# Kernel optimization log

Measured on AMD Instinct MI355X. Metric: run time of the kernel, lower is better.

## Reference

```python
import jax, jax.numpy as jnp
import numpy as np

N_NODES = 100000
N_EDGES = 600000
D = 128
BN_EPS = 1e-5


def setup_inputs() -> dict:
    key = jax.random.key(0)
    k = jax.random.split(key, 4)
    x = jax.random.normal(k[0], (N_NODES, D), dtype=jnp.float32)
    edge_index = jax.random.randint(k[1], (2, N_EDGES), 0, N_NODES, dtype=jnp.int32)
    W = jax.random.normal(k[2], (D, D), dtype=jnp.float32) * 0.05  # GCNConv weight
    b = jnp.zeros((D,), dtype=jnp.float32)                          # GCNConv bias
    gamma = jnp.ones((D,), dtype=jnp.float32)                       # BatchNorm weight
    beta = jnp.zeros((D,), dtype=jnp.float32)                       # BatchNorm bias
    return {"x": x, "edge_index": edge_index, "W": W, "b": b, "gamma": gamma, "beta": beta}


def reference(x, edge_index, W, b, gamma, beta):
    N = x.shape[0]
    # GCNConv: h = D^{-1/2} (A + I) D^{-1/2} (x W) + b
    h = x @ W  # [N, D]
    self_loops = jnp.arange(N, dtype=edge_index.dtype)
    src = jnp.concatenate([edge_index[0], self_loops])  # message source j
    dst = jnp.concatenate([edge_index[1], self_loops])  # aggregation target i
    deg = jax.ops.segment_sum(jnp.ones_like(dst, dtype=h.dtype), dst, num_segments=N)
    dinv = jax.lax.rsqrt(deg)  # deg >= 1 thanks to self-loops
    norm = dinv[src] * dinv[dst]  # [E+N]
    out = jax.ops.segment_sum(h[src] * norm[:, None], dst, num_segments=N) + b
    # BatchNorm (training-mode batch stats over nodes) + ReLU
    mean = jnp.mean(out, axis=0)
    var = jnp.mean((out - mean) ** 2, axis=0)
    out = (out - mean) * jax.lax.rsqrt(var + BN_EPS) * gamma + beta
    out = jax.nn.relu(out)
    # residual (in_ch == out_ch -> identity)
    return out + x
```

## Files before the change

kernel.cpp:

```cpp
#include <hip/hip_runtime.h>

#define NN 100000
#define NE 600000
#define DD 128
#define BN_EPS 1e-5f
#define NB1 391
#define NCV 12500
#define NFB 2344
#define NBLK 1563

typedef __attribute__((ext_vector_type(8))) short bf16x8;
typedef __attribute__((ext_vector_type(4))) float f32x4;

static __device__ __forceinline__ unsigned short f2bf(float f) {
    unsigned u = __float_as_uint(f);
    unsigned r = (u + 0x7FFFu + ((u >> 16) & 1u)) >> 16;
    return (unsigned short)r;
}
static __device__ __forceinline__ float bflo(unsigned v) { return __uint_as_float(v << 16); }
static __device__ __forceinline__ float bfhi(unsigned v) { return __uint_as_float(v & 0xFFFF0000u); }

__global__ __launch_bounds__(256) void k_init(int* __restrict__ cnt,
                                              float* __restrict__ stats,
                                              const float* __restrict__ W,
                                              unsigned short* __restrict__ Wt) {
    int i = blockIdx.x * 256 + threadIdx.x;
    if (i < NN) cnt[i] = 0;
    if (i < 256) stats[i] = 0.0f;
    if (i < DD * DD) {
        int k = i >> 7, c = i & 127;
        Wt[c * DD + k] = f2bf(W[i]);
    }
}

__global__ __launch_bounds__(256) void k_count(const int* __restrict__ dst,
                                               int* __restrict__ cnt) {
    int e = blockIdx.x * 256 + threadIdx.x;
    if (e < NE) atomicAdd(&cnt[dst[e]], 1);
}

__global__ __launch_bounds__(256) void k_scan1(const int* __restrict__ cnt,
                                               int* __restrict__ offs,
                                               int* __restrict__ bsum) {
    __shared__ int tmp[256];
    int tid = threadIdx.x;
    int i = blockIdx.x * 256 + tid;
    int v = (i < NN) ? (cnt[i] + 1) : 0;
    tmp[tid] = v;
    __syncthreads();
    #pragma unroll
    for (int d = 1; d < 256; d <<= 1) {
        int t = (tid >= d) ? tmp[tid - d] : 0;
        __syncthreads();
        tmp[tid] += t;
        __syncthreads();
    }
    if (i < NN) offs[i] = tmp[tid] - v;
    if (tid == 255) bsum[blockIdx.x] = tmp[255];
}

__global__ __launch_bounds__(512) void k_scan2(int* __restrict__ bsum) {
    __shared__ int tmp[512];
    int tid = threadIdx.x;
    int v = (tid < NB1) ? bsum[tid] : 0;
    tmp[tid] = v;
    __syncthreads();
    #pragma unroll
    for (int d = 1; d < 512; d <<= 1) {
        int t = (tid >= d) ? tmp[tid - d] : 0;
        __syncthreads();
        tmp[tid] += t;
        __syncthreads();
    }
    if (tid < NB1) bsum[tid] = tmp[tid] - v;
}

__global__ __launch_bounds__(256) void k_scan3(int* __restrict__ offs,
                                               const int* __restrict__ bsum,
                                               const int* __restrict__ cnt,
                                               int* __restrict__ cur,
                                               float* __restrict__ dinv,
                                               int* __restrict__ srcs) {
    int i = blockIdx.x * 256 + threadIdx.x;
    if (i < NN) {
        int o = offs[i] + bsum[blockIdx.x];
        offs[i] = o;
        dinv[i] = rsqrtf((float)(cnt[i] + 1));
        srcs[o] = i;
        cur[i]  = o + 1;
        if (i == 0) offs[NN] = NE + NN;
    }
}

__global__ __launch_bounds__(256) void k_cvfill(const float* __restrict__ x,
                                                const float* __restrict__ dinv,
                                                unsigned short* __restrict__ xn,
                                                const int* __restrict__ src,
                                                const int* __restrict__ dst,
                                                int* __restrict__ cur,
                                                int* __restrict__ srcs) {
    int bid = blockIdx.x;
    if (bid < NFB) {
        int e = bid * 256 + threadIdx.x;
        if (e < NE) {
            int s = src[e], t = dst[e];
            int slot = atomicAdd(&cur[t], 1);
            srcs[slot] = s;
        }
    } else {
        int r  = (bid - NFB) * 8 + (threadIdx.x >> 5);
        int c4 = threadIdx.x & 31;
        float di = dinv[r];
        float4 v = ((const float4*)x)[(size_t)r * 32 + c4];
        unsigned p0 = ((unsigned)f2bf(v.y * di) << 16) | f2bf(v.x * di);
        unsigned p1 = ((unsigned)f2bf(v.w * di) << 16) | f2bf(v.z * di);
        ((uint2*)xn)[(size_t)r * 32 + c4] = make_uint2(p0, p1);
    }
}

__global__ __launch_bounds__(256) void k_gather(const int* __restrict__ offs,
                                                const int* __restrict__ srcs,
                                                const unsigned short* __restrict__ xn,
                                                const float* __restrict__ dinv,
                                                const float* __restrict__ b,
                                                const unsigned short* __restrict__ Wt,
                                                float* __restrict__ out,
                                                float* __restrict__ partial) {
    __shared__ uint4 Wl4[2048];
    __shared__ float lsum[4][128], lss[4][128];
    const int tid  = threadIdx.x;
    const int wid  = tid >> 6;
    const int lane = tid & 63;
    const int lm   = lane & 15;
    const int lk   = lane >> 4;
    char* Wl = (char*)Wl4;

    #pragma unroll
    for (int it = 0; it < 8; ++it) {
        int chunk = it * 256 + tid;
        int row = chunk >> 4, c16 = chunk & 15;
        uint4 v = *(const uint4*)(Wt + row * DD + c16 * 8);
        *(uint4*)(Wl + row * 256 + ((c16 ^ (row & 7)) << 4)) = v;
    }
    float bb[8];
    #pragma unroll
    for (int nt = 0; nt < 8; ++nt) bb[nt] = b[nt * 16 + lm];
    __syncthreads();

    const int nbase = (blockIdx.x * 4 + wid) * 16;
    float s8[8], ss8[8];
    #pragma unroll
    for (int j = 0; j < 8; ++j) { s8[j] = 0.0f; ss8[j] = 0.0f; }

    if (nbase < NN) {
        int   ol = offs[nbase + (lane <= 16 ? lane : 16)];
        float dv = (lane < 16) ? dinv[nbase + lane] : 0.0f;
        int   beg = __shfl(ol, lm);
        int   n   = __shfl(ol, lm + 1) - beg;
        float di  = __shfl(dv, lm);
        const uint4* xn4 = (const uint4*)xn;

        float acc[4][8];
        #pragma unroll
        for (int ks = 0; ks < 4; ++ks)
            #pragma unroll
            for (int j = 0; j < 8; ++j) acc[ks][j] = 0.0f;

        int k = 0;
        for (; k + 2 <= n; k += 2) {
            int s0 = srcs[beg + k];
            int s1 = srcs[beg + k + 1];
            uint4 v0[4], v1[4];
            #pragma unroll
            for (int ks = 0; ks < 4; ++ks) v0[ks] = xn4[(size_t)s0 * 16 + ks * 4 + lk];
            #pragma unroll
            for (int ks = 0; ks < 4; ++ks) v1[ks] = xn4[(size_t)s1 * 16 + ks * 4 + lk];
            #pragma unroll
            for (int ks = 0; ks < 4; ++ks) {
                acc[ks][0] += bflo(v0[ks].x) + bflo(v1[ks].x);
                acc[ks][1] += bfhi(v0[ks].x) + bfhi(v1[ks].x);
                acc[ks][2] += bflo(v0[ks].y) + bflo(v1[ks].y);
                acc[ks][3] += bfhi(v0[ks].y) + bfhi(v1[ks].y);
                acc[ks][4] += bflo(v0[ks].z) + bflo(v1[ks].z);
                acc[ks][5] += bfhi(v0[ks].z) + bfhi(v1[ks].z);
                acc[ks][6] += bflo(v0[ks].w) + bflo(v1[ks].w);
                acc[ks][7] += bfhi(v0[ks].w) + bfhi(v1[ks].w);
            }
        }
        if (k < n) {
            int s0 = srcs[beg + k];
            #pragma unroll
            for (int ks = 0; ks < 4; ++ks) {
                uint4 v = xn4[(size_t)s0 * 16 + ks * 4 + lk];
                acc[ks][0] += bflo(v.x); acc[ks][1] += bfhi(v.x);
                acc[ks][2] += bflo(v.y); acc[ks][3] += bfhi(v.y);
                acc[ks][4] += bflo(v.z); acc[ks][5] += bfhi(v.z);
                acc[ks][6] += bflo(v.w); acc[ks][7] += bfhi(v.w);
            }
        }

        bf16x8 a[4];
        #pragma unroll
        for (int ks = 0; ks < 4; ++ks)
            #pragma unroll
            for (int j = 0; j < 8; ++j) a[ks][j] = (short)f2bf(acc[ks][j] * di);

        f32x4 dacc[8];
        #pragma unroll
        for (int nt = 0; nt < 8; ++nt) dacc[nt] = (f32x4){0.f, 0.f, 0.f, 0.f};
        #pragma unroll
        for (int ks = 0; ks < 4; ++ks)
            #pragma unroll
            for (int nt = 0; nt < 8; ++nt) {
                int brow = nt * 16 + lm;
                bf16x8 bfr = *(const bf16x8*)(Wl + brow * 256 + ((ks * 64 + lk * 16) ^ ((brow & 7) << 4)));
                dacc[nt] = __builtin_amdgcn_mfma_f32_16x16x32_bf16(a[ks], bfr, dacc[nt], 0, 0, 0);
            }

        #pragma unroll
        for (int nt = 0; nt < 8; ++nt)
            #pragma unroll
            for (int r = 0; r < 4; ++r) {
                float val = dacc[nt][r] + bb[nt];
                out[(size_t)(nbase + lk * 4 + r) * DD + nt * 16 + lm] = val;
                s8[nt] += val; ss8[nt] += val * val;
            }
    }

    #pragma unroll
    for (int nt = 0; nt < 8; ++nt) {
        s8[nt]  += __shfl_xor(s8[nt], 16);  s8[nt]  += __shfl_xor(s8[nt], 32);
        ss8[nt] += __shfl_xor(ss8[nt], 16); ss8[nt] += __shfl_xor(ss8[nt], 32);
    }
    if (lk == 0) {
        #pragma unroll
        for (int nt = 0; nt < 8; ++nt) {
            lsum[wid][nt * 16 + lm] = s8[nt];
            lss[wid][nt * 16 + lm]  = ss8[nt];
        }
    }
    __syncthreads();
    if (tid < 128) {
        float a = lsum[0][tid] + lsum[1][tid] + lsum[2][tid] + lsum[3][tid];
        float c = lss[0][tid]  + lss[1][tid]  + lss[2][tid]  + lss[3][tid];
        partial[(size_t)blockIdx.x * 256 + tid]       = a;
        partial[(size_t)blockIdx.x * 256 + 128 + tid] = c;
    }
}

__global__ __launch_bounds__(256) void k_red(const float* __restrict__ partial,
                                             float* __restrict__ stats) {
    int tid = threadIdx.x;
    float a = 0.0f;
    for (int r = blockIdx.x; r < NBLK; r += 64)
        a += partial[(size_t)r * 256 + tid];
    unsafeAtomicAdd(&stats[tid], a);
}

__global__ __launch_bounds__(256) void k_final(float* __restrict__ out,
                                               const float* __restrict__ x,
                                               const float* __restrict__ gamma,
                                               const float* __restrict__ beta,
                                               const float* __restrict__ stats) {
    int idx = blockIdx.x * 256 + threadIdx.x;
    if (idx >= NN * DD / 4) return;
    int c4 = idx & 31;

    const float invN = 1.0f / (float)NN;
    float4 sm  = ((const float4*)stats)[c4];
    float4 sq  = ((const float4*)stats)[32 + c4];
    float4 g   = ((const float4*)gamma)[c4];
    float4 be  = ((const float4*)beta)[c4];
    float4 v   = ((float4*)out)[idx];
    float4 xr  = ((const float4*)x)[idx];

    float m0 = sm.x * invN, m1 = sm.y * invN, m2 = sm.z * invN, m3 = sm.w * invN;
    float r0 = rsqrtf(sq.x * invN - m0 * m0 + BN_EPS);
    float r1 = rsqrtf(sq.y * invN - m1 * m1 + BN_EPS);
    float r2 = rsqrtf(sq.z * invN - m2 * m2 + BN_EPS);
    float r3 = rsqrtf(sq.w * invN - m3 * m3 + BN_EPS);

    float4 o;
    o.x = fmaxf((v.x - m0) * r0 * g.x + be.x, 0.0f) + xr.x;
    o.y = fmaxf((v.y - m1) * r1 * g.y + be.y, 0.0f) + xr.y;
    o.z = fmaxf((v.z - m2) * r2 * g.z + be.z, 0.0f) + xr.z;
    o.w = fmaxf((v.w - m3) * r3 * g.w + be.w, 0.0f) + xr.w;
    ((float4*)out)[idx] = o;
}

extern "C" void kernel_launch(void* const* d_in, const int* in_sizes, int n_in,
                              void* d_out, int out_size, void* d_ws, size_t ws_size,
                              hipStream_t stream) {
    const float* x     = (const float*)d_in[0];
    const int*   ei    = (const int*)d_in[1];
    const float* W     = (const float*)d_in[2];
    const float* b     = (const float*)d_in[3];
    const float* gamma = (const float*)d_in[4];
    const float* beta  = (const float*)d_in[5];
    float*       out   = (float*)d_out;

    char*  base = (char*)d_ws;
    size_t off  = 0;
    auto carve = [&](size_t bytes) -> void* {
        void* p = base + off;
        off = (off + bytes + 255) & ~(size_t)255;
        return p;
    };
    unsigned short* xn    = (unsigned short*)carve((size_t)NN * DD * 2);
    float*          dinv  = (float*)carve((size_t)NN * 4);
    float*          stats = (float*)carve(256 * 4);
    int*            cnt   = (int*)carve((size_t)NN * 4);
    int*            offs  = (int*)carve((size_t)(NN + 1) * 4);
    int*            cur   = (int*)carve((size_t)NN * 4);
    int*            bsum  = (int*)carve(2048);
    int*            srcs  = (int*)carve((size_t)(NE + NN) * 4);
    unsigned short* Wt    = (unsigned short*)carve(DD * DD * 2);
    float*          partial = (float*)carve((size_t)NBLK * 256 * 4);

    const int* src = ei;
    const int* dst = ei + NE;

    k_init   <<<NB1, 256, 0, stream>>>(cnt, stats, W, Wt);
    k_count  <<<(NE + 255) / 256, 256, 0, stream>>>(dst, cnt);
    k_scan1  <<<NB1, 256, 0, stream>>>(cnt, offs, bsum);
    k_scan2  <<<1, 512, 0, stream>>>(bsum);
    k_scan3  <<<NB1, 256, 0, stream>>>(offs, bsum, cnt, cur, dinv, srcs);
    k_cvfill <<<NFB + NCV, 256, 0, stream>>>(x, dinv, xn, src, dst, cur, srcs);
    k_gather <<<NBLK, 256, 0, stream>>>(offs, srcs, xn, dinv, b, Wt, out, partial);
    k_red    <<<64, 256, 0, stream>>>(partial, stats);
    k_final  <<<(NN * DD / 4 + 255) / 256, 256, 0, stream>>>(out, x, gamma, beta, stats);
}
```

Measured before the change: 159.3 us.

## Use persistent dynamic tile scheduling in gather and precompute edge ranks for CSR fill

The gather kernel becomes persistent: 1280 blocks whose waves pull 16-node tiles from a global atomic counter until all tiles are done. This is meant to balance uneven degree distributions and cut the number of per-block W-tile loads into LDS. The count kernel now records each edge's rank from its degree atomic, so the CSR fill writes slots directly without a second atomic pass. That removes the cur array but adds a rank array write and read. The stats scratch reuses the W LDS buffer behind an extra barrier.

```diff
diff --git a/kernel.cpp b/kernel.cpp
--- a/kernel.cpp
+++ b/kernel.cpp
@@ -7,7 +7,8 @@
 #define NB1 391
 #define NCV 12500
 #define NFB 2344
-#define NBLK 1563
+#define NBLK 1280
+#define NTILES 6250
 
 typedef __attribute__((ext_vector_type(8))) short bf16x8;
 typedef __attribute__((ext_vector_type(4))) float f32x4;
@@ -22,11 +23,13 @@
 
 __global__ __launch_bounds__(256) void k_init(int* __restrict__ cnt,
                                               float* __restrict__ stats,
+                                              int* __restrict__ ctr,
                                               const float* __restrict__ W,
                                               unsigned short* __restrict__ Wt) {
     int i = blockIdx.x * 256 + threadIdx.x;
     if (i < NN) cnt[i] = 0;
     if (i < 256) stats[i] = 0.0f;
+    if (i == 0) *ctr = 0;
     if (i < DD * DD) {
         int k = i >> 7, c = i & 127;
         Wt[c * DD + k] = f2bf(W[i]);
@@ -34,9 +37,10 @@
 }
 
 __global__ __launch_bounds__(256) void k_count(const int* __restrict__ dst,
-                                               int* __restrict__ cnt) {
+                                               int* __restrict__ cnt,
+                                               int* __restrict__ rank) {
     int e = blockIdx.x * 256 + threadIdx.x;
-    if (e < NE) atomicAdd(&cnt[dst[e]], 1);
+    if (e < NE) rank[e] = atomicAdd(&cnt[dst[e]], 1);
 }
 
 __global__ __launch_bounds__(256) void k_scan1(const int* __restrict__ cnt,
@@ -78,7 +82,6 @@
 __global__ __launch_bounds__(256) void k_scan3(int* __restrict__ offs,
                                                const int* __restrict__ bsum,
                                                const int* __restrict__ cnt,
-                                               int* __restrict__ cur,
                                                float* __restrict__ dinv,
                                                int* __restrict__ srcs) {
     int i = blockIdx.x * 256 + threadIdx.x;
@@ -87,7 +90,6 @@
         offs[i] = o;
         dinv[i] = rsqrtf((float)(cnt[i] + 1));
         srcs[o] = i;
-        cur[i]  = o + 1;
         if (i == 0) offs[NN] = NE + NN;
     }
 }
@@ -97,15 +99,15 @@
                                                 unsigned short* __restrict__ xn,
                                                 const int* __restrict__ src,
                                                 const int* __restrict__ dst,
-                                                int* __restrict__ cur,
+                                                const int* __restrict__ rank,
+                                                const int* __restrict__ offs,
                                                 int* __restrict__ srcs) {
     int bid = blockIdx.x;
     if (bid < NFB) {
         int e = bid * 256 + threadIdx.x;
         if (e < NE) {
-            int s = src[e], t = dst[e];
-            int slot = atomicAdd(&cur[t], 1);
-            srcs[slot] = s;
+            int t = dst[e];
+            srcs[offs[t] + 1 + rank[e]] = src[e];
         }
     } else {
         int r  = (bid - NFB) * 8 + (threadIdx.x >> 5);
@@ -124,10 +126,10 @@
                                                 const float* __restrict__ dinv,
                                                 const float* __restrict__ b,
                                                 const unsigned short* __restrict__ Wt,
+                                                int* __restrict__ ctr,
                                                 float* __restrict__ out,
                                                 float* __restrict__ partial) {
     __shared__ uint4 Wl4[2048];
-    __shared__ float lsum[4][128], lss[4][128];
     const int tid  = threadIdx.x;
     const int wid  = tid >> 6;
     const int lane = tid & 63;
@@ -147,18 +149,23 @@
     for (int nt = 0; nt < 8; ++nt) bb[nt] = b[nt * 16 + lm];
     __syncthreads();
 
-    const int nbase = (blockIdx.x * 4 + wid) * 16;
     float s8[8], ss8[8];
     #pragma unroll
     for (int j = 0; j < 8; ++j) { s8[j] = 0.0f; ss8[j] = 0.0f; }
-
-    if (nbase < NN) {
+    const uint4* xn4 = (const uint4*)xn;
+
+    for (;;) {
+        int tile = 0;
+        if (lane == 0) tile = atomicAdd(ctr, 1);
+        tile = __shfl(tile, 0);
+        if (tile >= NTILES) break;
+        const int nbase = tile * 16;
+
         int   ol = offs[nbase + (lane <= 16 ? lane : 16)];
         float dv = (lane < 16) ? dinv[nbase + lane] : 0.0f;
         int   beg = __shfl(ol, lm);
         int   n   = __shfl(ol, lm + 1) - beg;
         float di  = __shfl(dv, lm);
-        const uint4* xn4 = (const uint4*)xn;
 
         float acc[4][8];
         #pragma unroll
@@ -232,17 +239,19 @@
         s8[nt]  += __shfl_xor(s8[nt], 16);  s8[nt]  += __shfl_xor(s8[nt], 32);
         ss8[nt] += __shfl_xor(ss8[nt], 16); ss8[nt] += __shfl_xor(ss8[nt], 32);
     }
+    __syncthreads();
+    float* sp = (float*)Wl4;
     if (lk == 0) {
         #pragma unroll
         for (int nt = 0; nt < 8; ++nt) {
-            lsum[wid][nt * 16 + lm] = s8[nt];
-            lss[wid][nt * 16 + lm]  = ss8[nt];
+            sp[wid * 128 + nt * 16 + lm]       = s8[nt];
+            sp[512 + wid * 128 + nt * 16 + lm] = ss8[nt];
         }
     }
     __syncthreads();
     if (tid < 128) {
-        float a = lsum[0][tid] + lsum[1][tid] + lsum[2][tid] + lsum[3][tid];
-        float c = lss[0][tid]  + lss[1][tid]  + lss[2][tid]  + lss[3][tid];
+        float a = sp[tid] + sp[128 + tid] + sp[256 + tid] + sp[384 + tid];
+        float c = sp[512 + tid] + sp[640 + tid] + sp[768 + tid] + sp[896 + tid];
         partial[(size_t)blockIdx.x * 256 + tid]       = a;
         partial[(size_t)blockIdx.x * 256 + 128 + tid] = c;
     }
@@ -311,22 +320,23 @@
     float*          stats = (float*)carve(256 * 4);
     int*            cnt   = (int*)carve((size_t)NN * 4);
     int*            offs  = (int*)carve((size_t)(NN + 1) * 4);
-    int*            cur   = (int*)carve((size_t)NN * 4);
+    int*            rank  = (int*)carve((size_t)NE * 4);
     int*            bsum  = (int*)carve(2048);
     int*            srcs  = (int*)carve((size_t)(NE + NN) * 4);
     unsigned short* Wt    = (unsigned short*)carve(DD * DD * 2);
+    int*            ctr   = (int*)carve(256);
     float*          partial = (float*)carve((size_t)NBLK * 256 * 4);
 
     const int* src = ei;
     const int* dst = ei + NE;
 
-    k_init   <<<NB1, 256, 0, stream>>>(cnt, stats, W, Wt);
-    k_count  <<<(NE + 255) / 256, 256, 0, stream>>>(dst, cnt);
+    k_init   <<<NB1, 256, 0, stream>>>(cnt, stats, ctr, W, Wt);
+    k_count  <<<(NE + 255) / 256, 256, 0, stream>>>(dst, cnt, rank);
     k_scan1  <<<NB1, 256, 0, stream>>>(cnt, offs, bsum);
     k_scan2  <<<1, 512, 0, stream>>>(bsum);
-    k_scan3  <<<NB1, 256, 0, stream>>>(offs, bsum, cnt, cur, dinv, srcs);
-    k_cvfill <<<NFB + NCV, 256, 0, stream>>>(x, dinv, xn, src, dst, cur, srcs);
-    k_gather <<<NBLK, 256, 0, stream>>>(offs, srcs, xn, dinv, b, Wt, out, partial);
+    k_scan3  <<<NB1, 256, 0, stream>>>(offs, bsum, cnt, dinv, srcs);
+    k_cvfill <<<NFB + NCV, 256, 0, stream>>>(x, dinv, xn, src, dst, rank, offs, srcs);
+    k_gather <<<NBLK, 256, 0, stream>>>(offs, srcs, xn, dinv, b, Wt, ctr, out, partial);
     k_red    <<<64, 256, 0, stream>>>(partial, stats);
     k_final  <<<(NN * DD / 4 + 255) / 256, 256, 0, stream>>>(out, x, gamma, beta, stats);
 }
```

Result: slower. 235.6 us (+47.9%).
